# Kernel tuning notes

Hardware: AMD Instinct MI355X
Metric: run time of the kernel (lower is better)

## Reference

```python
import jax, jax.numpy as jnp
import numpy as np

NUM_CODES = 4096
TEMPERATURE = 1.0
EPS = 1e-08


def setup_inputs() -> dict:
    key = jax.random.key(0)
    k1, k2, k3 = jax.random.split(key, 3)
    B, D, T = 16, 512, 1500
    encoder_stride = 320
    student_features = jax.random.normal(k1, (B, D, T), dtype=jnp.float32)
    codebook = jax.random.normal(k2, (NUM_CODES, D), dtype=jnp.float32)
    lengths = jax.random.randint(k3, (B,), 0, T * encoder_stride, dtype=jnp.int64)
    return {
        "student_features": student_features,
        "codebook": codebook,
        "lengths": lengths,
        "encoder_stride": encoder_stride,
    }


def _length_mask(lengths, T, stride):
    # frame t is valid iff t < floor(length / stride)  -> (B, T) float mask
    n_valid = jnp.minimum(lengths // stride, T)
    return (jnp.arange(T)[None, :] < n_valid[:, None]).astype(jnp.float32)


def reference(student_features, codebook, lengths, encoder_stride):
    B, D, T = student_features.shape
    mask = _length_mask(lengths, T, encoder_stride)            # (B, T)
    z = jnp.transpose(student_features, (0, 2, 1)).reshape(-1, D)  # (N, D), N = B*T
    # Euclidean cdist via ||z||^2 + ||c||^2 - 2 z c^T (same as torch.cdist GEMM path)
    z2 = jnp.sum(z * z, axis=-1, keepdims=True)                # (N, 1)
    c2 = jnp.sum(codebook * codebook, axis=-1)                 # (K,)
    d2 = z2 + c2[None, :] - 2.0 * (z @ codebook.T)             # (N, K)
    distances = jnp.sqrt(jnp.maximum(d2, 1e-12))
    logits = -distances / TEMPERATURE
    probs = jax.nn.softmax(logits, axis=-1)                    # (N, K)
    probs_masked = probs * mask.reshape(-1, 1)
    code_dist = jnp.sum(probs_masked, axis=0)                  # (K,)
    code_dist = code_dist / (jnp.sum(code_dist) + EPS)
    entropy = -jnp.sum(code_dist * jnp.log(code_dist + EPS))
    max_entropy = jnp.log(jnp.float32(NUM_CODES))
    return 1.0 - entropy / max_entropy
```

## Files before the change

kernel.cpp:

```cpp
#include <hip/hip_runtime.h>
#include <hip/hip_bf16.h>

#define NUM_B   16
#define DIM     512
#define TT      1500
#define NROWS   (NUM_B * TT)
#define NCODES  4096
#define ROW_TILES ((NROWS + 127) / 128)
#define NROWS_PAD (ROW_TILES * 128)
#define NSLICE  8
#define SHIFTC  30.0f
#define NBLKX   (NCODES / 128)
#define TBLKS   (NUM_B * 47)
#define CBLKS   (NCODES / 4)
#define NZERO   (NROWS_PAD + NSLICE * NCODES)
#define NZERO2  (NZERO + 1)

typedef __bf16 bf16x8 __attribute__((ext_vector_type(8)));
typedef float  floatx4 __attribute__((ext_vector_type(4)));
typedef unsigned short ushortx8 __attribute__((ext_vector_type(8)));

__device__ __forceinline__ void glds16(const void* g, void* l) {
    __builtin_amdgcn_global_load_lds(
        (__attribute__((address_space(1))) void*)(void*)g,
        (__attribute__((address_space(3))) void*)l, 16, 0, 0);
}

__global__ __launch_bounds__(256) void k_prep(
    const float* __restrict__ sf, const float* __restrict__ cb,
    unsigned short* __restrict__ zbf, unsigned short* __restrict__ cbbf,
    float* __restrict__ z2, float* __restrict__ c2, float* __restrict__ zero0,
    float* __restrict__ outp) {
    int id = blockIdx.x, tid = threadIdx.x;
    if (id < TBLKS) {
        __shared__ float tile[32][257];
        int b = id / 47, t0 = (id % 47) * 32;
        int tl = tid & 31, dg = tid >> 5;
        int tr = tid >> 3, dgr = tid & 7;
        int tg = t0 + tr;
        float ssq = 0.f;
        unsigned short* dst = zbf + (size_t)(b * TT + tg) * DIM;
#pragma unroll
        for (int half = 0; half < 2; ++half) {
            int dbase = half * 256;
            if (half) __syncthreads();
            int t = t0 + tl;
            if (t < TT) {
                const float* src = sf + (size_t)(b * DIM + dbase + dg * 32) * TT + t;
#pragma unroll
                for (int k = 0; k < 32; ++k)
                    tile[tl][dg * 32 + k] = src[(size_t)k * TT];
            }
            __syncthreads();
            if (tg < TT) {
#pragma unroll
                for (int seg = 0; seg < 4; ++seg) {
                    int d0 = seg * 64 + dgr * 8;
                    unsigned int h[8];
#pragma unroll
                    for (int i2 = 0; i2 < 8; ++i2) {
                        __hip_bfloat16 hb = __float2bfloat16(tile[tr][d0 + i2]);
                        h[i2] = __builtin_bit_cast(unsigned short, hb);
                        float vb = __bfloat162float(hb);
                        ssq += vb * vb;
                    }
                    uint4 o;
                    o.x = h[0] | (h[1] << 16); o.y = h[2] | (h[3] << 16);
                    o.z = h[4] | (h[5] << 16); o.w = h[6] | (h[7] << 16);
                    *(uint4*)(dst + dbase + d0) = o;
                }
            }
        }
        ssq += __shfl_xor(ssq, 1); ssq += __shfl_xor(ssq, 2); ssq += __shfl_xor(ssq, 4);
        if (dgr == 0 && tg < TT) z2[b * TT + tg] = ssq;
    } else {
        int ci = id - TBLKS;
        int gid = ci * 256 + tid;
        if (gid < NZERO2) zero0[gid] = 0.f;
        if (ci == 0 && tid == 0) outp[0] = 1.0f;
        int k = ci * 4 + (tid >> 6);
        int lane = tid & 63;
        const float4* src = (const float4*)(cb + (size_t)k * DIM + lane * 8);
        float4 a = src[0], b2 = src[1];
        float vals[8] = {a.x, a.y, a.z, a.w, b2.x, b2.y, b2.z, b2.w};
        float s = 0.f;
        unsigned int h[8];
#pragma unroll
        for (int i = 0; i < 8; ++i) {
            __hip_bfloat16 hb = __float2bfloat16(vals[i]);
            h[i] = __builtin_bit_cast(unsigned short, hb);
            float vb = __bfloat162float(hb);
            s += vb * vb;
        }
        uint4 o;
        o.x = h[0] | (h[1] << 16); o.y = h[2] | (h[3] << 16);
        o.z = h[4] | (h[5] << 16); o.w = h[6] | (h[7] << 16);
        *(uint4*)(cbbf + (size_t)k * DIM + lane * 8) = o;
#pragma unroll
        for (int off = 32; off >= 1; off >>= 1) s += __shfl_down(s, off);
        if (lane == 0) c2[k] = s;
    }
}

__global__ __launch_bounds__(256, 2) void k_gemm1(
    const unsigned short* __restrict__ zbf, const unsigned short* __restrict__ cbbf,
    const float* __restrict__ z2, const float* __restrict__ c2,
    const int* __restrict__ lengths, const int* __restrict__ stride_p,
    float* __restrict__ Sg, unsigned short* __restrict__ Eg) {
    __shared__ unsigned short As[128 * 64];
    __shared__ unsigned short Bs[128 * 64];
    __shared__ float z2s[128], c2s[128];
    __shared__ unsigned char vldp[128];
    __shared__ int s_any;
    int tid = threadIdx.x;
    int r0 = blockIdx.y * 128, c0 = blockIdx.x * 128;
    if (tid == 0) s_any = 0;
    __syncthreads();
    if (tid < 128) {
        int n = r0 + tid;
        int valid = 0;
        if (n < NROWS) {
            int b = n / TT, t = n - b * TT;
            int stride = stride_p[0];
            int nv = lengths[b] / stride;
            if (nv > TT) nv = TT;
            valid = (t < nv);
        }
        if (valid) atomicOr(&s_any, 1);
        vldp[tid] = (unsigned char)valid;
        z2s[tid] = z2[r0 + tid];
        c2s[tid] = c2[c0 + tid];
    }
    __syncthreads();
    if (!s_any) return;

    int wave = tid >> 6, lane = tid & 63;
    int l15 = lane & 15, l4 = lane >> 4;
    int wr = (wave >> 1) * 64, wc = (wave & 1) * 64;

    int srow = lane >> 3;
    int scg = (lane & 7) ^ srow;
    const unsigned short* ag = zbf + (size_t)(r0 + wave * 32 + srow) * DIM + scg * 8;
    const unsigned short* bg = cbbf + (size_t)(c0 + wave * 32 + srow) * DIM + scg * 8;
    unsigned short* al = As + (wave * 32) * 64;
    unsigned short* bl = Bs + (wave * 32) * 64;

    floatx4 acc[4][4];
    const floatx4 zero = {0.f, 0.f, 0.f, 0.f};
#pragma unroll
    for (int i = 0; i < 4; ++i)
#pragma unroll
        for (int j = 0; j < 4; ++j) acc[i][j] = zero;

    int sw = l15 & 7;

    for (int kc = 0; kc < 8; ++kc) {
#pragma unroll
        for (int q = 0; q < 4; ++q) {
            glds16(ag + (size_t)q * 8 * DIM + kc * 64, al + q * 8 * 64);
            glds16(bg + (size_t)q * 8 * DIM + kc * 64, bl + q * 8 * 64);
        }
        __syncthreads();
#pragma unroll
        for (int ks = 0; ks < 64; ks += 32) {
            int g = (ks >> 3) + l4;
            int pcg = g ^ sw;
            bf16x8 av[4], bv[4];
#pragma unroll
            for (int i = 0; i < 4; ++i)
                av[i] = __builtin_bit_cast(bf16x8,
                    *(const ushortx8*)&As[(wr + 16 * i + l15) * 64 + pcg * 8]);
#pragma unroll
            for (int j = 0; j < 4; ++j)
                bv[j] = __builtin_bit_cast(bf16x8,
                    *(const ushortx8*)&Bs[(wc + 16 * j + l15) * 64 + pcg * 8]);
#pragma unroll
            for (int i = 0; i < 4; ++i)
#pragma unroll
                for (int j = 0; j < 4; ++j)
                    acc[i][j] = __builtin_amdgcn_mfma_f32_16x16x32_bf16(bv[j], av[i], acc[i][j], 0, 0, 0);
        }
        __syncthreads();
    }

    float c2r[4][4];
#pragma unroll
    for (int j = 0; j < 4; ++j)
#pragma unroll
        for (int r = 0; r < 4; ++r)
            c2r[j][r] = c2s[wc + 16 * j + 4 * l4 + r];

#pragma unroll
    for (int i = 0; i < 4; ++i) {
        int rl = wr + 16 * i + l15;
        bool rv = vldp[rl] != 0;
        float z2v = z2s[rl];
        float s = 0.f;
        unsigned short* Ep = Eg + (size_t)(r0 + rl) * NCODES + c0 + wc + l4 * 4;
#pragma unroll
        for (int j = 0; j < 4; ++j) {
            float e[4];
#pragma unroll
            for (int r = 0; r < 4; ++r) {
                float d2 = z2v + c2r[j][r] - 2.0f * acc[i][j][r];
                float d = sqrtf(fmaxf(d2, 1e-12f));
                e[r] = __expf(SHIFTC - d);
                s += e[r];
            }
            if (rv) {
                unsigned h0 = __builtin_bit_cast(unsigned short, __float2bfloat16(e[0]));
                unsigned h1 = __builtin_bit_cast(unsigned short, __float2bfloat16(e[1]));
                unsigned h2 = __builtin_bit_cast(unsigned short, __float2bfloat16(e[2]));
                unsigned h3 = __builtin_bit_cast(unsigned short, __float2bfloat16(e[3]));
                uint2 o;
                o.x = h0 | (h1 << 16);
                o.y = h2 | (h3 << 16);
                *(uint2*)(Ep + 16 * j) = o;
            }
        }
        s += __shfl_xor(s, 16); s += __shfl_xor(s, 32);
        if (l4 == 0 && rv) atomicAdd(&Sg[r0 + rl], s);
    }
}

__global__ __launch_bounds__(256) void k_scan(
    const unsigned short* __restrict__ Eg, const float* __restrict__ Sg,
    const int* __restrict__ lengths, const int* __restrict__ stride_p,
    float* __restrict__ cdp) {
    __shared__ float rs2[64];
    __shared__ unsigned char vrows[64];
    __shared__ int s_cnt;
    int tid = threadIdx.x;
    int r0 = blockIdx.y * 64;
    if (tid < 64) {
        int valid = 0;
        float inv = 0.f;
        int n = r0 + tid;
        if (n < NROWS) {
            int b = n / TT, t = n - b * TT;
            int nv = lengths[b] / stride_p[0];
            if (nv > TT) nv = TT;
            valid = (t < nv);
            if (valid) inv = 1.0f / Sg[n];
        }
        unsigned long long mask = __ballot(valid);
        if (tid == 0) s_cnt = __popcll(mask);
        if (valid) {
            int pos = __popcll(mask & ((1ull << tid) - 1ull));
            vrows[pos] = (unsigned char)tid;
            rs2[pos] = inv;
        }
    }
    __syncthreads();
    int m = s_cnt;
    if (m == 0) return;

    int col0 = blockIdx.x * 1024 + tid * 4;
    const unsigned short* base = Eg + (size_t)r0 * NCODES + col0;
    float acc[4] = {0.f, 0.f, 0.f, 0.f};

#define ACC4(V, RN) do { \
    unsigned int _u[2] = {(V).x, (V).y}; \
    _Pragma("unroll") \
    for (int q = 0; q < 2; ++q) { \
        acc[2 * q]     += (RN) * __builtin_bit_cast(float, _u[q] << 16); \
        acc[2 * q + 1] += (RN) * __builtin_bit_cast(float, _u[q] & 0xffff0000u); \
    } \
} while (0)

    int i = 0;
    for (; i + 8 <= m; i += 8) {
        uint2 v0 = *(const uint2*)(base + (size_t)vrows[i]     * NCODES);
        uint2 v1 = *(const uint2*)(base + (size_t)vrows[i + 1] * NCODES);
        uint2 v2 = *(const uint2*)(base + (size_t)vrows[i + 2] * NCODES);
        uint2 v3 = *(const uint2*)(base + (size_t)vrows[i + 3] * NCODES);
        uint2 v4 = *(const uint2*)(base + (size_t)vrows[i + 4] * NCODES);
        uint2 v5 = *(const uint2*)(base + (size_t)vrows[i + 5] * NCODES);
        uint2 v6 = *(const uint2*)(base + (size_t)vrows[i + 6] * NCODES);
        uint2 v7 = *(const uint2*)(base + (size_t)vrows[i + 7] * NCODES);
        ACC4(v0, rs2[i]);     ACC4(v1, rs2[i + 1]);
        ACC4(v2, rs2[i + 2]); ACC4(v3, rs2[i + 3]);
        ACC4(v4, rs2[i + 4]); ACC4(v5, rs2[i + 5]);
        ACC4(v6, rs2[i + 6]); ACC4(v7, rs2[i + 7]);
    }
    for (; i < m; ++i) {
        uint2 v = *(const uint2*)(base + (size_t)vrows[i] * NCODES);
        ACC4(v, rs2[i]);
    }
#undef ACC4

    float* outp = cdp + (size_t)(blockIdx.y & (NSLICE - 1)) * NCODES;
#pragma unroll
    for (int t = 0; t < 4; ++t) atomicAdd(&outp[col0 + t], acc[t]);
}

template <int PASS>
__global__ __launch_bounds__(256, 2) void k_gemm(
    const unsigned short* __restrict__ zbf, const unsigned short* __restrict__ cbbf,
    const float* __restrict__ z2, const float* __restrict__ c2,
    const int* __restrict__ lengths, const int* __restrict__ stride_p,
    float* __restrict__ Sg, float* __restrict__ cd) {
    __shared__ unsigned short Asf[128 * 64];
    __shared__ unsigned short Bsf[128 * 64];
    __shared__ float z2s[128], c2s[128], rs[128];
    __shared__ int s_any;
    int tid = threadIdx.x;
    int r0 = blockIdx.y * 128, c0 = blockIdx.x * 128;
    if (tid == 0) s_any = 0;
    __syncthreads();
    if (tid < 128) {
        int n = r0 + tid;
        int valid = 0;
        if (n < NROWS) {
            int b = n / TT, t = n - b * TT;
            int stride = stride_p[0];
            int nv = lengths[b] / stride;
            if (nv > TT) nv = TT;
            valid = (t < nv);
        }
        if (valid) atomicOr(&s_any, 1);
        z2s[tid] = z2[r0 + tid];
        c2s[tid] = c2[c0 + tid];
        if (PASS == 2) rs[tid] = valid ? (1.0f / Sg[r0 + tid]) : 0.0f;
    }
    __syncthreads();
    if (!s_any) return;

    int wave = tid >> 6, lane = tid & 63;
    int l15 = lane & 15, l4 = lane >> 4;
    int wr = (wave >> 1) * 64, wc = (wave & 1) * 64;
    int srow = lane >> 3;
    int scg = (lane & 7) ^ srow;
    const unsigned short* ag = zbf + (size_t)(r0 + wave * 32 + srow) * DIM + scg * 8;
    const unsigned short* bg = cbbf + (size_t)(c0 + wave * 32 + srow) * DIM + scg * 8;
    unsigned short* al = Asf + (wave * 32) * 64;
    unsigned short* bl = Bsf + (wave * 32) * 64;

    floatx4 acc[4][4];
    const floatx4 zero = {0.f, 0.f, 0.f, 0.f};
#pragma unroll
    for (int i = 0; i < 4; ++i)
#pragma unroll
        for (int j = 0; j < 4; ++j) acc[i][j] = zero;
    int sw = l15 & 7;
    for (int kc = 0; kc < 8; ++kc) {
#pragma unroll
        for (int q = 0; q < 4; ++q) {
            glds16(ag + (size_t)q * 8 * DIM + kc * 64, al + q * 8 * 64);
            glds16(bg + (size_t)q * 8 * DIM + kc * 64, bl + q * 8 * 64);
        }
        __syncthreads();
#pragma unroll
        for (int ks = 0; ks < 64; ks += 32) {
            int g = (ks >> 3) + l4;
            int pcg = g ^ sw;
            bf16x8 av[4], bvv[4];
#pragma unroll
            for (int i = 0; i < 4; ++i)
                av[i] = __builtin_bit_cast(bf16x8, *(const ushortx8*)&Asf[(wr + 16 * i + l15) * 64 + pcg * 8]);
#pragma unroll
            for (int j = 0; j < 4; ++j)
                bvv[j] = __builtin_bit_cast(bf16x8, *(const ushortx8*)&Bsf[(wc + 16 * j + l15) * 64 + pcg * 8]);
#pragma unroll
            for (int i = 0; i < 4; ++i)
#pragma unroll
                for (int j = 0; j < 4; ++j)
                    acc[i][j] = __builtin_amdgcn_mfma_f32_16x16x32_bf16(av[i], bvv[j], acc[i][j], 0, 0, 0);
        }
        __syncthreads();
    }
    if (PASS == 1) {
#pragma unroll
        for (int i = 0; i < 4; ++i) {
#pragma unroll
            for (int r = 0; r < 4; ++r) {
                int rl = wr + 16 * i + 4 * l4 + r;
                float z2v = z2s[rl];
                float s = 0.f;
#pragma unroll
                for (int j = 0; j < 4; ++j) {
                    int cl = wc + 16 * j + l15;
                    float d2 = z2v + c2s[cl] - 2.0f * acc[i][j][r];
                    float d = sqrtf(fmaxf(d2, 1e-12f));
                    s += __expf(SHIFTC - d);
                }
                s += __shfl_xor(s, 1); s += __shfl_xor(s, 2);
                s += __shfl_xor(s, 4); s += __shfl_xor(s, 8);
                if (l15 == 0) atomicAdd(&Sg[r0 + rl], s);
            }
        }
    } else {
#pragma unroll
        for (int j = 0; j < 4; ++j) {
            int cl = wc + 16 * j + l15;
            float c2v = c2s[cl];
            float cs = 0.f;
#pragma unroll
            for (int i = 0; i < 4; ++i) {
#pragma unroll
                for (int r = 0; r < 4; ++r) {
                    int rl = wr + 16 * i + 4 * l4 + r;
                    float d2 = z2s[rl] + c2v - 2.0f * acc[i][j][r];
                    float d = sqrtf(fmaxf(d2, 1e-12f));
                    cs += __expf(SHIFTC - d) * rs[rl];
                }
            }
            cs += __shfl_xor(cs, 16); cs += __shfl_xor(cs, 32);
            if (l4 == 0) atomicAdd(&cd[c0 + cl], cs);
        }
    }
}

__global__ __launch_bounds__(256) void k_red(float* __restrict__ cdp,
                                             float* __restrict__ tot) {
    int k = blockIdx.x * 256 + threadIdx.x;
    float v = 0.f;
#pragma unroll
    for (int s = 0; s < NSLICE; ++s) v += cdp[(size_t)s * NCODES + k];
    cdp[k] = v;
    float t = v;
#pragma unroll
    for (int off = 32; off >= 1; off >>= 1) t += __shfl_down(t, off);
    if ((threadIdx.x & 63) == 0) atomicAdd(tot, t);
}

__global__ __launch_bounds__(256) void k_ent(const float* __restrict__ cdp,
                                             const float* __restrict__ tot,
                                             float* __restrict__ out) {
    int k = blockIdx.x * 256 + threadIdx.x;
    float inv = 1.0f / (tot[0] + 1e-8f);
    float p = cdp[k] * inv;
    float e = p * __logf(p + 1e-8f);
#pragma unroll
    for (int off = 32; off >= 1; off >>= 1) e += __shfl_down(e, off);
    if ((threadIdx.x & 63) == 0)
        atomicAdd(out, e * (1.0f / __logf((float)NCODES)));
}

extern "C" void kernel_launch(void* const* d_in, const int* in_sizes, int n_in,
                              void* d_out, int out_size, void* d_ws, size_t ws_size,
                              hipStream_t stream) {
    const float* sf = (const float*)d_in[0];
    const float* cb = (const float*)d_in[1];
    const int* lengths = (const int*)d_in[2];
    const int* stride_p = (const int*)d_in[3];

    float* wsf = (float*)d_ws;
    float* Sg = wsf;
    float* cdp = Sg + NROWS_PAD;
    float* tot = wsf + NZERO;
    const size_t OFF_Z2 = NZERO2;
    const size_t OFF_C2 = OFF_Z2 + NROWS_PAD;
    const size_t OFF_ZB = (OFF_C2 + NCODES + 3) & ~(size_t)3;
    float* z2 = wsf + OFF_Z2;
    float* c2 = wsf + OFF_C2;
    unsigned short* zbf = (unsigned short*)(wsf + OFF_ZB);
    unsigned short* cbbf = zbf + (size_t)NROWS_PAD * DIM;
    unsigned short* Eg = cbbf + (size_t)NCODES * DIM;

    size_t need = OFF_ZB * 4
                + ((size_t)NROWS_PAD * DIM + (size_t)NCODES * DIM
                 + (size_t)NROWS_PAD * NCODES) * 2;

    k_prep<<<dim3(TBLKS + CBLKS), 256, 0, stream>>>(
        sf, cb, zbf, cbbf, z2, c2, Sg, (float*)d_out);
    if (ws_size >= need) {
        k_gemm1<<<dim3(NBLKX, ROW_TILES), 256, 0, stream>>>(
            zbf, cbbf, z2, c2, lengths, stride_p, Sg, Eg);
        k_scan<<<dim3(4, NROWS_PAD / 64), 256, 0, stream>>>(
            Eg, Sg, lengths, stride_p, cdp);
    } else {
        k_gemm<1><<<dim3(NBLKX, ROW_TILES), 256, 0, stream>>>(zbf, cbbf, z2, c2, lengths, stride_p, Sg, cdp);
        k_gemm<2><<<dim3(NBLKX, ROW_TILES), 256, 0, stream>>>(zbf, cbbf, z2, c2, lengths, stride_p, Sg, cdp);
    }
    k_red<<<dim3(NCODES / 256), 256, 0, stream>>>(cdp, tot);
    k_ent<<<dim3(NCODES / 256), 256, 0, stream>>>(cdp, tot, (float*)d_out);
}
```

Before: 217.9 us.

## Stride rows across scan blocks so each block gets balanced valid-row load

```diff
diff --git a/kernel.cpp b/kernel.cpp
--- a/kernel.cpp
+++ b/kernel.cpp
@@ -15,6 +15,7 @@
 #define CBLKS   (NCODES / 4)
 #define NZERO   (NROWS_PAD + NSLICE * NCODES)
 #define NZERO2  (NZERO + 1)
+#define RPB     188
 
 typedef __bf16 bf16x8 __attribute__((ext_vector_type(8)));
 typedef float  floatx4 __attribute__((ext_vector_type(4)));
@@ -227,36 +228,41 @@
     const unsigned short* __restrict__ Eg, const float* __restrict__ Sg,
     const int* __restrict__ lengths, const int* __restrict__ stride_p,
     float* __restrict__ cdp) {
-    __shared__ float rs2[64];
-    __shared__ unsigned char vrows[64];
-    __shared__ int s_cnt;
+    __shared__ float rs2[RPB];
+    __shared__ unsigned char vrows[RPB];
+    __shared__ int wtot[4];
     int tid = threadIdx.x;
-    int r0 = blockIdx.y * 64;
-    if (tid < 64) {
-        int valid = 0;
-        float inv = 0.f;
-        int n = r0 + tid;
+    int y0 = blockIdx.y;
+    int lane = tid & 63, wv = tid >> 6;
+
+    int valid = 0;
+    float inv = 0.f;
+    if (tid < RPB) {
+        int n = y0 + 128 * tid;
         if (n < NROWS) {
             int b = n / TT, t = n - b * TT;
             int nv = lengths[b] / stride_p[0];
             if (nv > TT) nv = TT;
-            valid = (t < nv);
-            if (valid) inv = 1.0f / Sg[n];
-        }
-        unsigned long long mask = __ballot(valid);
-        if (tid == 0) s_cnt = __popcll(mask);
-        if (valid) {
-            int pos = __popcll(mask & ((1ull << tid) - 1ull));
-            vrows[pos] = (unsigned char)tid;
-            rs2[pos] = inv;
-        }
-    }
-    __syncthreads();
-    int m = s_cnt;
+            if (t < nv) { valid = 1; inv = 1.0f / Sg[n]; }
+        }
+    }
+    unsigned long long mask = __ballot(valid);
+    if (lane == 0) wtot[wv] = __popcll(mask);
+    __syncthreads();
+    int base = 0;
+#pragma unroll
+    for (int w = 0; w < 4; ++w) if (w < wv) base += wtot[w];
+    if (valid) {
+        int pos = base + __popcll(mask & ((1ull << lane) - 1ull));
+        vrows[pos] = (unsigned char)tid;
+        rs2[pos] = inv;
+    }
+    __syncthreads();
+    int m = wtot[0] + wtot[1] + wtot[2] + wtot[3];
     if (m == 0) return;
 
     int col0 = blockIdx.x * 1024 + tid * 4;
-    const unsigned short* base = Eg + (size_t)r0 * NCODES + col0;
+    const unsigned short* base_e = Eg + col0;
     float acc[4] = {0.f, 0.f, 0.f, 0.f};
 
 #define ACC4(V, RN) do { \
@@ -268,25 +274,27 @@
     } \
 } while (0)
 
+#define ROWP(I) (base_e + (size_t)(y0 + 128 * (int)vrows[I]) * NCODES)
     int i = 0;
     for (; i + 8 <= m; i += 8) {
-        uint2 v0 = *(const uint2*)(base + (size_t)vrows[i]     * NCODES);
-        uint2 v1 = *(const uint2*)(base + (size_t)vrows[i + 1] * NCODES);
-        uint2 v2 = *(const uint2*)(base + (size_t)vrows[i + 2] * NCODES);
-        uint2 v3 = *(const uint2*)(base + (size_t)vrows[i + 3] * NCODES);
-        uint2 v4 = *(const uint2*)(base + (size_t)vrows[i + 4] * NCODES);
-        uint2 v5 = *(const uint2*)(base + (size_t)vrows[i + 5] * NCODES);
-        uint2 v6 = *(const uint2*)(base + (size_t)vrows[i + 6] * NCODES);
-        uint2 v7 = *(const uint2*)(base + (size_t)vrows[i + 7] * NCODES);
+        uint2 v0 = *(const uint2*)ROWP(i);
+        uint2 v1 = *(const uint2*)ROWP(i + 1);
+        uint2 v2 = *(const uint2*)ROWP(i + 2);
+        uint2 v3 = *(const uint2*)ROWP(i + 3);
+        uint2 v4 = *(const uint2*)ROWP(i + 4);
+        uint2 v5 = *(const uint2*)ROWP(i + 5);
+        uint2 v6 = *(const uint2*)ROWP(i + 6);
+        uint2 v7 = *(const uint2*)ROWP(i + 7);
         ACC4(v0, rs2[i]);     ACC4(v1, rs2[i + 1]);
         ACC4(v2, rs2[i + 2]); ACC4(v3, rs2[i + 3]);
         ACC4(v4, rs2[i + 4]); ACC4(v5, rs2[i + 5]);
         ACC4(v6, rs2[i + 6]); ACC4(v7, rs2[i + 7]);
     }
     for (; i < m; ++i) {
-        uint2 v = *(const uint2*)(base + (size_t)vrows[i] * NCODES);
+        uint2 v = *(const uint2*)ROWP(i);
         ACC4(v, rs2[i]);
     }
+#undef ROWP
 #undef ACC4
 
     float* outp = cdp + (size_t)(blockIdx.y & (NSLICE - 1)) * NCODES;
@@ -467,7 +475,7 @@
     if (ws_size >= need) {
         k_gemm1<<<dim3(NBLKX, ROW_TILES), 256, 0, stream>>>(
             zbf, cbbf, z2, c2, lengths, stride_p, Sg, Eg);
-        k_scan<<<dim3(4, NROWS_PAD / 64), 256, 0, stream>>>(
+        k_scan<<<dim3(4, 128), 256, 0, stream>>>(
             Eg, Sg, lengths, stride_p, cdp);
     } else {
         k_gemm<1><<<dim3(NBLKX, ROW_TILES), 256, 0, stream>>>(zbf, cbbf, z2, c2, lengths, stride_p, Sg, cdp);
```

New measurement: 217.3 us. About the same (-0.3%).
